# Kernel tuning notes

Measured on AMD Instinct MI355X. Metric: run time of the kernel, lower is better.

## Reference

```python
import jax, jax.numpy as jnp
import numpy as np

LAM = 1.0
POLY_K = 3

B, M, D = 4, 50000, 8
E = 1600000


def setup_inputs() -> dict:
    key = jax.random.key(0)
    k1, k2, k3, k4, k5, k6 = jax.random.split(key, 6)
    c0 = jax.random.normal(k1, (B, M, D), dtype=jnp.float32)
    src = jax.random.randint(k2, (E,), 0, M, dtype=jnp.int32)
    dst = jax.random.randint(k3, (E,), 0, M, dtype=jnp.int32)
    # scale restriction maps down so (lam*L)^k stays numerically sane for k<=3
    R_src = jax.random.normal(k4, (E, D, D), dtype=jnp.float32) * 0.1
    R_dst = jax.random.normal(k5, (E, D, D), dtype=jnp.float32) * 0.1
    poly_coeffs = jax.random.normal(k6, (POLY_K + 1,), dtype=jnp.float32)
    return {"c0": c0, "src": src, "dst": dst, "R_src": R_src,
            "R_dst": R_dst, "poly_coeffs": poly_coeffs}


def _laplace_acc(p, src, dst, R_src, R_dst):
    # p: [B, M, d]; R_*: [E, a, d]; src/dst: [E]
    p_src = p[:, src, :]                                  # [B, E, d] gather
    p_dst = p[:, dst, :]                                  # [B, E, d]
    tmp_src = jnp.einsum('ead,bed->bea', R_src, p_src)    # [B, E, a]
    tmp_dst = jnp.einsum('ead,bed->bea', R_dst, p_dst)
    r = tmp_src - tmp_dst                                 # edge residual
    c_src = jnp.einsum('ead,bea->bed', R_src, r)          # [B, E, d]
    c_dst = -jnp.einsum('ead,bea->bed', R_dst, r)
    acc = jnp.zeros_like(p)
    acc = acc.at[:, src, :].add(c_src)                    # scatter-add to nodes
    acc = acc.at[:, dst, :].add(c_dst)
    return acc


def reference(c0, src, dst, R_src, R_dst, poly_coeffs):
    # monomial basis, poly_norm='none': out = sum_k a_k (lam L)^k c0
    out = poly_coeffs[0] * c0
    v = c0
    for k in range(1, POLY_K + 1):
        v = LAM * _laplace_acc(v, src, dst, R_src, R_dst)
        out = out + poly_coeffs[k] * v
    return out
```

## Files before the change

### kernel.cpp

```cpp
#include <hip/hip_runtime.h>


#define BLOCK 256

__global__ __launch_bounds__(BLOCK) void edge_kernel(
    const float* __restrict__ p,
    const int*   __restrict__ src,
    const int*   __restrict__ dst,
    const float* __restrict__ Rs,
    const float* __restrict__ Rd,
    float*       __restrict__ acc,
    int E, int M)
{
    long tid = (long)blockIdx.x * BLOCK + threadIdx.x;
    int e = (int)(tid >> 5);
    if (e >= E) return;
    int lane = (int)tid & 31;
    int t = lane & 7;
    int b = lane >> 3;

    int s = src[e];
    int d = dst[e];

    const float* rs = Rs + (size_t)e * 64 + t * 8;
    const float* rd = Rd + (size_t)e * 64 + t * 8;
    float4 rs0 = *(const float4*)(rs);
    float4 rs1 = *(const float4*)(rs + 4);
    float4 rd0 = *(const float4*)(rd);
    float4 rd1 = *(const float4*)(rd + 4);

    const float* ps = p + ((size_t)b * M + s) * 8;
    const float* pd = p + ((size_t)b * M + d) * 8;
    float4 ps0 = *(const float4*)(ps);
    float4 ps1 = *(const float4*)(ps + 4);
    float4 pd0 = *(const float4*)(pd);
    float4 pd1 = *(const float4*)(pd + 4);

    float r = rs0.x * ps0.x + rs0.y * ps0.y + rs0.z * ps0.z + rs0.w * ps0.w
            + rs1.x * ps1.x + rs1.y * ps1.y + rs1.z * ps1.z + rs1.w * ps1.w
            - rd0.x * pd0.x - rd0.y * pd0.y - rd0.z * pd0.z - rd0.w * pd0.w
            - rd1.x * pd1.x - rd1.y * pd1.y - rd1.z * pd1.z - rd1.w * pd1.w;

    const float* colS = Rs + (size_t)e * 64 + t;
    const float* colD = Rd + (size_t)e * 64 + t;
    float cs = 0.f, cd = 0.f;
#pragma unroll
    for (int a = 0; a < 8; a++) {
        float ra = __shfl(r, a, 8);
        cs += colS[a * 8] * ra;
        cd += colD[a * 8] * ra;
    }

    atomicAdd(acc + ((size_t)b * M + s) * 8 + t, cs);
    atomicAdd(acc + ((size_t)b * M + d) * 8 + t, -cd);
}

__global__ __launch_bounds__(BLOCK) void init_out_kernel(
    const float4* __restrict__ c0, const float* __restrict__ poly,
    float4* __restrict__ out, int n4)
{
    int i = blockIdx.x * BLOCK + threadIdx.x;
    if (i >= n4) return;
    float a = poly[0];
    float4 c = c0[i];
    out[i] = make_float4(a * c.x, a * c.y, a * c.z, a * c.w);
}

__global__ __launch_bounds__(BLOCK) void axpy_kernel(
    const float4* __restrict__ v, const float* __restrict__ poly, int k,
    float4* __restrict__ out, int n4)
{
    int i = blockIdx.x * BLOCK + threadIdx.x;
    if (i >= n4) return;
    float a = poly[k];
    float4 vv = v[i];
    float4 o = out[i];
    out[i] = make_float4(o.x + a * vv.x, o.y + a * vv.y,
                         o.z + a * vv.z, o.w + a * vv.w);
}

extern "C" void kernel_launch(void* const* d_in, const int* in_sizes, int n_in,
                              void* d_out, int out_size, void* d_ws, size_t ws_size,
                              hipStream_t stream) {
    const float* c0   = (const float*)d_in[0];
    const int*   src  = (const int*)d_in[1];
    const int*   dst  = (const int*)d_in[2];
    const float* Rs   = (const float*)d_in[3];
    const float* Rd   = (const float*)d_in[4];
    const float* poly = (const float*)d_in[5];
    float* out = (float*)d_out;

    const int B = 4, D = 8;
    const int E = in_sizes[1];
    const int M = in_sizes[0] / (B * D);
    const size_t nElem = (size_t)B * M * D;
    const int n4 = (int)(nElem / 4);

    float* bufA = (float*)d_ws;
    float* bufB = bufA + nElem;

    init_out_kernel<<<(n4 + BLOCK - 1) / BLOCK, BLOCK, 0, stream>>>(
        (const float4*)c0, poly, (float4*)out, n4);

    const float* p = c0;
    float* accs[3] = { bufA, bufB, bufA };
    long nEdgeThreads = (long)E * 32;
    int edgeBlocks = (int)((nEdgeThreads + BLOCK - 1) / BLOCK);

    for (int k = 1; k <= 3; k++) {
        float* acc = accs[k - 1];
        hipMemsetAsync(acc, 0, nElem * sizeof(float), stream);
        edge_kernel<<<edgeBlocks, BLOCK, 0, stream>>>(p, src, dst, Rs, Rd, acc, E, M);
        axpy_kernel<<<(n4 + BLOCK - 1) / BLOCK, BLOCK, 0, stream>>>(
            (const float4*)acc, poly, k, (float4*)out, n4);
        p = acc;
    }
}
```

Before: 2.507 ms.

## Replace atomic edge scatter with CSR node-centric gather and fused axpy

Builds a per-node incidence list (histogram, scan, fill) each launch, then runs a node-centric gather kernel where one wave per node accumulates contributions from all incident edges and reduces via shuffles. The polynomial accumulation into out is fused into the gather kernel, removing memsets, float atomics and separate axpy kernels. Costs a CSR build per call and reading each edge's restriction maps twice (once per endpoint), and a serial single-block scan.

```diff
diff --git a/kernel.cpp b/kernel.cpp
--- a/kernel.cpp
+++ b/kernel.cpp
@@ -3,80 +3,156 @@
 
 #define BLOCK 256
 
-__global__ __launch_bounds__(BLOCK) void edge_kernel(
+__global__ __launch_bounds__(BLOCK) void hist_kernel(
+    const int* __restrict__ src, const int* __restrict__ dst,
+    int* __restrict__ cnt, int E)
+{
+    int i = blockIdx.x * BLOCK + threadIdx.x;
+    if (i >= E) return;
+    atomicAdd(&cnt[src[i]], 1);
+    atomicAdd(&cnt[dst[i]], 1);
+}
+
+__global__ __launch_bounds__(BLOCK) void scan_kernel(
+    const int* __restrict__ cnt, int* __restrict__ off, int* __restrict__ cur, int M)
+{
+    __shared__ int sums[BLOCK];
+    int tid = threadIdx.x;
+    int chunk = (M + BLOCK - 1) / BLOCK;
+    int lo = tid * chunk;
+    int hi = lo + chunk; if (hi > M) hi = M;
+    int s = 0;
+    for (int i = lo; i < hi; i++) s += cnt[i];
+    sums[tid] = s;
+    __syncthreads();
+    if (tid == 0) {
+        int run = 0;
+        for (int i = 0; i < BLOCK; i++) { int v = sums[i]; sums[i] = run; run += v; }
+    }
+    __syncthreads();
+    int run = sums[tid];
+    for (int i = lo; i < hi; i++) {
+        int v = cnt[i];
+        off[i] = run;
+        cur[i] = run;
+        run += v;
+    }
+}
+
+__global__ __launch_bounds__(BLOCK) void fill_kernel(
+    const int* __restrict__ src, const int* __restrict__ dst,
+    int* __restrict__ cur, int2* __restrict__ idx, int E)
+{
+    int i = blockIdx.x * BLOCK + threadIdx.x;
+    if (i >= E) return;
+    int s = src[i], d = dst[i];
+    int ps = atomicAdd(&cur[s], 1);
+    idx[ps] = make_int2(i << 1, d);
+    int pd = atomicAdd(&cur[d], 1);
+    idx[pd] = make_int2((i << 1) | 1, s);
+}
+
+__global__ __launch_bounds__(BLOCK) void gather_kernel(
     const float* __restrict__ p,
-    const int*   __restrict__ src,
-    const int*   __restrict__ dst,
-    const float* __restrict__ Rs,
-    const float* __restrict__ Rd,
-    float*       __restrict__ acc,
-    int E, int M)
+    const float* __restrict__ Rs, const float* __restrict__ Rd,
+    const int* __restrict__ off, const int* __restrict__ endo,
+    const int2* __restrict__ idx,
+    const float* __restrict__ poly, int k,
+    const float* __restrict__ c0,
+    float* __restrict__ acc, float* __restrict__ out,
+    int M)
 {
-    long tid = (long)blockIdx.x * BLOCK + threadIdx.x;
-    int e = (int)(tid >> 5);
-    if (e >= E) return;
-    int lane = (int)tid & 31;
-    int t = lane & 7;
-    int b = lane >> 3;
+    int gw = (int)((blockIdx.x * BLOCK + threadIdx.x) >> 6);
+    if (gw >= M) return;
+    int m = gw;
+    int lane = threadIdx.x & 63;
+    int slot = lane >> 5;
+    int b = (lane >> 3) & 3;
+    int a = lane & 7;
 
-    int s = src[e];
-    int d = dst[e];
+    const float* pbase = p + (size_t)b * M * 8;
+    const float* pm = pbase + (size_t)m * 8;
+    float4 m0 = *(const float4*)pm;
+    float4 m1 = *(const float4*)(pm + 4);
 
-    const float* rs = Rs + (size_t)e * 64 + t * 8;
-    const float* rd = Rd + (size_t)e * 64 + t * 8;
-    float4 rs0 = *(const float4*)(rs);
-    float4 rs1 = *(const float4*)(rs + 4);
-    float4 rd0 = *(const float4*)(rd);
-    float4 rd1 = *(const float4*)(rd + 4);
+    float av0 = 0.f, av1 = 0.f, av2 = 0.f, av3 = 0.f;
+    float av4 = 0.f, av5 = 0.f, av6 = 0.f, av7 = 0.f;
 
-    const float* ps = p + ((size_t)b * M + s) * 8;
-    const float* pd = p + ((size_t)b * M + d) * 8;
-    float4 ps0 = *(const float4*)(ps);
-    float4 ps1 = *(const float4*)(ps + 4);
-    float4 pd0 = *(const float4*)(pd);
-    float4 pd1 = *(const float4*)(pd + 4);
+    int s0 = off[m];
+    int s1 = endo[m];
+    int arow = a * 8;
 
-    float r = rs0.x * ps0.x + rs0.y * ps0.y + rs0.z * ps0.z + rs0.w * ps0.w
-            + rs1.x * ps1.x + rs1.y * ps1.y + rs1.z * ps1.z + rs1.w * ps1.w
-            - rd0.x * pd0.x - rd0.y * pd0.y - rd0.z * pd0.z - rd0.w * pd0.w
-            - rd1.x * pd1.x - rd1.y * pd1.y - rd1.z * pd1.z - rd1.w * pd1.w;
+    for (int it = s0 + slot; it < s1; it += 2) {
+        int2 en = idx[it];
+        int e = en.x >> 1;
+        bool isDst = (en.x & 1) != 0;
+        int other = en.y;
 
-    const float* colS = Rs + (size_t)e * 64 + t;
-    const float* colD = Rd + (size_t)e * 64 + t;
-    float cs = 0.f, cd = 0.f;
-#pragma unroll
-    for (int a = 0; a < 8; a++) {
-        float ra = __shfl(r, a, 8);
-        cs += colS[a * 8] * ra;
-        cd += colD[a * 8] * ra;
+        const float* rp = Rs + (size_t)e * 64 + arow;
+        float4 A0 = *(const float4*)rp;
+        float4 A1 = *(const float4*)(rp + 4);
+        const float* dp = Rd + (size_t)e * 64 + arow;
+        float4 B0 = *(const float4*)dp;
+        float4 B1 = *(const float4*)(dp + 4);
+        const float* po = pbase + (size_t)other * 8;
+        float4 P0 = *(const float4*)po;
+        float4 P1 = *(const float4*)(po + 4);
+
+        float rAm = A0.x*m0.x + A0.y*m0.y + A0.z*m0.z + A0.w*m0.w
+                  + A1.x*m1.x + A1.y*m1.y + A1.z*m1.z + A1.w*m1.w;
+        float rAP = A0.x*P0.x + A0.y*P0.y + A0.z*P0.z + A0.w*P0.w
+                  + A1.x*P1.x + A1.y*P1.y + A1.z*P1.z + A1.w*P1.w;
+        float rBm = B0.x*m0.x + B0.y*m0.y + B0.z*m0.z + B0.w*m0.w
+                  + B1.x*m1.x + B1.y*m1.y + B1.z*m1.z + B1.w*m1.w;
+        float rBP = B0.x*P0.x + B0.y*P0.y + B0.z*P0.z + B0.w*P0.w
+                  + B1.x*P1.x + B1.y*P1.y + B1.z*P1.z + B1.w*P1.w;
+
+        float r  = isDst ? (rAP - rBm) : (rAm - rBP);
+        float rr = isDst ? -r : r;
+
+        av0 += (isDst ? B0.x : A0.x) * rr;
+        av1 += (isDst ? B0.y : A0.y) * rr;
+        av2 += (isDst ? B0.z : A0.z) * rr;
+        av3 += (isDst ? B0.w : A0.w) * rr;
+        av4 += (isDst ? B1.x : A1.x) * rr;
+        av5 += (isDst ? B1.y : A1.y) * rr;
+        av6 += (isDst ? B1.z : A1.z) * rr;
+        av7 += (isDst ? B1.w : A1.w) * rr;
     }
 
-    atomicAdd(acc + ((size_t)b * M + s) * 8 + t, cs);
-    atomicAdd(acc + ((size_t)b * M + d) * 8 + t, -cd);
-}
+    av0 += __shfl_xor(av0, 32);
+    av1 += __shfl_xor(av1, 32);
+    av2 += __shfl_xor(av2, 32);
+    av3 += __shfl_xor(av3, 32);
+    av4 += __shfl_xor(av4, 32);
+    av5 += __shfl_xor(av5, 32);
+    av6 += __shfl_xor(av6, 32);
+    av7 += __shfl_xor(av7, 32);
 
-__global__ __launch_bounds__(BLOCK) void init_out_kernel(
-    const float4* __restrict__ c0, const float* __restrict__ poly,
-    float4* __restrict__ out, int n4)
-{
-    int i = blockIdx.x * BLOCK + threadIdx.x;
-    if (i >= n4) return;
-    float a = poly[0];
-    float4 c = c0[i];
-    out[i] = make_float4(a * c.x, a * c.y, a * c.z, a * c.w);
-}
+    bool h4 = (a & 4) != 0;
+    float k0 = h4 ? av4 : av0, q0 = h4 ? av0 : av4;
+    float k1 = h4 ? av5 : av1, q1 = h4 ? av1 : av5;
+    float k2 = h4 ? av6 : av2, q2 = h4 ? av2 : av6;
+    float k3 = h4 ? av7 : av3, q3 = h4 ? av3 : av7;
+    float w0 = k0 + __shfl_xor(q0, 4);
+    float w1 = k1 + __shfl_xor(q1, 4);
+    float w2 = k2 + __shfl_xor(q2, 4);
+    float w3 = k3 + __shfl_xor(q3, 4);
+    bool h2 = (a & 2) != 0;
+    float t0 = h2 ? w2 : w0, u0 = h2 ? w0 : w2;
+    float t1 = h2 ? w3 : w1, u1 = h2 ? w1 : w3;
+    float x0 = t0 + __shfl_xor(u0, 2);
+    float x1 = t1 + __shfl_xor(u1, 2);
+    bool h1 = (a & 1) != 0;
+    float yk = h1 ? x1 : x0, ys = h1 ? x0 : x1;
+    float val = yk + __shfl_xor(ys, 1);
 
-__global__ __launch_bounds__(BLOCK) void axpy_kernel(
-    const float4* __restrict__ v, const float* __restrict__ poly, int k,
-    float4* __restrict__ out, int n4)
-{
-    int i = blockIdx.x * BLOCK + threadIdx.x;
-    if (i >= n4) return;
-    float a = poly[k];
-    float4 vv = v[i];
-    float4 o = out[i];
-    out[i] = make_float4(o.x + a * vv.x, o.y + a * vv.y,
-                         o.z + a * vv.z, o.w + a * vv.w);
+    if (lane < 32) {
+        size_t o = ((size_t)b * M + m) * 8 + a;
+        acc[o] = val;
+        float base = (k == 1) ? poly[0] * c0[o] : out[o];
+        out[o] = base + poly[k] * val;
+    }
 }
 
 extern "C" void kernel_launch(void* const* d_in, const int* in_sizes, int n_in,
@@ -94,25 +170,23 @@
     const int E = in_sizes[1];
     const int M = in_sizes[0] / (B * D);
     const size_t nElem = (size_t)B * M * D;
-    const int n4 = (int)(nElem / 4);
 
     float* bufA = (float*)d_ws;
     float* bufB = bufA + nElem;
+    int2*  idx  = (int2*)(bufB + nElem);
+    int*   cnt  = (int*)(idx + (size_t)2 * E);
+    int*   off  = cnt + M;
+    int*   cur  = off + M;
 
-    init_out_kernel<<<(n4 + BLOCK - 1) / BLOCK, BLOCK, 0, stream>>>(
-        (const float4*)c0, poly, (float4*)out, n4);
+    hipMemsetAsync(cnt, 0, (size_t)M * sizeof(int), stream);
+    int eb = (E + BLOCK - 1) / BLOCK;
+    hist_kernel<<<eb, BLOCK, 0, stream>>>(src, dst, cnt, E);
+    scan_kernel<<<1, BLOCK, 0, stream>>>(cnt, off, cur, M);
+    fill_kernel<<<eb, BLOCK, 0, stream>>>(src, dst, cur, idx, E);
 
-    const float* p = c0;
-    float* accs[3] = { bufA, bufB, bufA };
-    long nEdgeThreads = (long)E * 32;
-    int edgeBlocks = (int)((nEdgeThreads + BLOCK - 1) / BLOCK);
-
-    for (int k = 1; k <= 3; k++) {
-        float* acc = accs[k - 1];
-        hipMemsetAsync(acc, 0, nElem * sizeof(float), stream);
-        edge_kernel<<<edgeBlocks, BLOCK, 0, stream>>>(p, src, dst, Rs, Rd, acc, E, M);
-        axpy_kernel<<<(n4 + BLOCK - 1) / BLOCK, BLOCK, 0, stream>>>(
-            (const float4*)acc, poly, k, (float4*)out, n4);
-        p = acc;
-    }
+    long nThreads = (long)M * 64;
+    int gb = (int)((nThreads + BLOCK - 1) / BLOCK);
+    gather_kernel<<<gb, BLOCK, 0, stream>>>(c0,   Rs, Rd, off, cur, idx, poly, 1, c0, bufA, out, M);
+    gather_kernel<<<gb, BLOCK, 0, stream>>>(bufA, Rs, Rd, off, cur, idx, poly, 2, c0, bufB, out, M);
+    gather_kernel<<<gb, BLOCK, 0, stream>>>(bufB, Rs, Rd, off, cur, idx, poly, 3, c0, bufA, out, M);
 }
```

New measurement: 2.658 ms. 1.06x slower.
